# Optimization experiments

Hardware: AMD Instinct MI355X
Metric: run time of the kernel (lower is better)

## Reference

```python
import jax, jax.numpy as jnp
import numpy as np

# dims: heads, batch, seq (== maxSentenceSize), embed, key/query dim, value dim
H, B, S, E, DK, DV = 16, 4, 1024, 1024, 64, 64
SCALE = int(np.sqrt(DK))  # original uses int(np.sqrt(keySize)) == 8


def setup_inputs() -> dict:
    key = jax.random.key(0)
    k = jax.random.split(key, 5)
    embeddings = jax.random.normal(k[0], (B, S, E), jnp.float32)
    # original init: uniform(0, 1) weights
    Wq = jax.random.uniform(k[1], (H, E, DK), jnp.float32)
    Wk = jax.random.uniform(k[2], (H, E, DK), jnp.float32)
    # note: original valueWeights are also sized (E, keySize)
    Wv = jax.random.uniform(k[3], (H, E, DK), jnp.float32)
    Wo = jax.random.uniform(k[4], (H * DV, E), jnp.float32)
    return {"embeddings": embeddings, "Wq": Wq, "Wk": Wk, "Wv": Wv, "Wo": Wo}


def _causal_mask(s):
    # 0 on/below diagonal, -inf above (matches the torch list-comprehension mask)
    return jnp.where(jnp.tril(jnp.ones((s, s), bool)), 0.0, -jnp.inf).astype(jnp.float32)


def reference(embeddings, Wq, Wk, Wv, Wo):
    # per-head projections, all heads batched: [H,B,S,d]
    q = jnp.einsum('bse,hed->hbsd', embeddings, Wq)
    kk = jnp.einsum('bse,hed->hbsd', embeddings, Wk)
    v = jnp.einsum('bse,hed->hbsd', embeddings, Wv)
    # FAITHFUL to original: keys are RESHAPED (flat reinterpretation [S,DK]->[DK,S]
    # per (head,batch) slice), NOT transposed.
    kT = kk.reshape(H, B, DK, S)
    mask = _causal_mask(S)  # [S,S]
    # softmax((QK_reshaped + mask) / int(sqrt(keySize)))
    scores = (jnp.einsum('hbsd,hbdt->hbst', q, kT) + mask) / SCALE
    attn = jax.nn.softmax(scores, axis=-1)  # [H,B,S,S]
    av = jnp.einsum('hbst,hbtd->hbsd', attn, v)  # [H,B,S,DV]
    # FAITHFUL to original: flat reshape [H,B,S,DV] -> [B,S,DV*H]
    concat = av.reshape(B, S, DV * H)
    return concat @ Wo  # [B,S,E]
```

## Files before the change

### kernel.cpp

```cpp
#include <hip/hip_runtime.h>
#include <math.h>

#define H 16
#define B 4
#define S 1024
#define E 1024
#define DK 64

typedef _Float16 f16x8 __attribute__((ext_vector_type(8)));
typedef _Float16 f16x4 __attribute__((ext_vector_type(4)));
typedef float    f32x4 __attribute__((ext_vector_type(4)));

__device__ __forceinline__ int swzb(int row, int colByte) {
    return row * 128 + (colByte ^ ((row & 7) << 4));
}

__global__ __launch_bounds__(256) void cvt_split_emb(const float* __restrict__ in,
                                                     _Float16* __restrict__ outH,
                                                     _Float16* __restrict__ outL) {
    int i = (blockIdx.x * 256 + threadIdx.x) * 8;
    float4 a = *(const float4*)&in[i];
    float4 b = *(const float4*)&in[i + 4];
    float x[8] = {a.x, a.y, a.z, a.w, b.x, b.y, b.z, b.w};
    f16x8 h, l;
    #pragma unroll
    for (int j = 0; j < 8; ++j) {
        _Float16 hh = (_Float16)x[j];
        h[j] = hh;
        l[j] = (_Float16)(x[j] - (float)hh);
    }
    *(f16x8*)&outH[i] = h;
    *(f16x8*)&outL[i] = l;
}

__global__ __launch_bounds__(256) void cvt_weights(
    const float* __restrict__ Wq, const float* __restrict__ Wk,
    const float* __restrict__ Wv, const float* __restrict__ Wo,
    _Float16* __restrict__ WTh, _Float16* __restrict__ WTl,
    _Float16* __restrict__ WoT) {
    __shared__ _Float16 Th[64 * 64];
    __shared__ _Float16 Tl[64 * 64];
    int tid = threadIdx.x;
    if (blockIdx.y < 48) {
        int et = blockIdx.x, chunk = blockIdx.y;
        const float* W = (chunk < 16 ? Wq : chunk < 32 ? Wk : Wv)
                         + (size_t)(chunk & 15) * E * DK;
        #pragma unroll
        for (int rr = 0; rr < 4; ++rr) {
            int u = rr * 256 + tid;
            int ei = u >> 4, f4 = u & 15;
            float4 v = *(const float4*)&W[(size_t)(et * 64 + ei) * 64 + f4 * 4];
            float x[4] = {v.x, v.y, v.z, v.w};
            f16x4 h, l;
            #pragma unroll
            for (int j = 0; j < 4; ++j) {
                _Float16 hh = (_Float16)x[j];
                h[j] = hh;
                l[j] = (_Float16)(x[j] - (float)hh);
            }
            *(f16x4*)((char*)Th + swzb(ei, f4 * 8)) = h;
            *(f16x4*)((char*)Tl + swzb(ei, f4 * 8)) = l;
        }
        __syncthreads();
        #pragma unroll
        for (int rr = 0; rr < 2; ++rr) {
            int u = rr * 256 + tid;
            int d = u >> 3, e8 = u & 7;
            f16x8 oh, ol;
            #pragma unroll
            for (int j = 0; j < 8; ++j) {
                int ei = e8 * 8 + j;
                oh[j] = *(_Float16*)((char*)Th + swzb(ei, d * 2));
                ol[j] = *(_Float16*)((char*)Tl + swzb(ei, d * 2));
            }
            size_t idx = (size_t)(chunk * 64 + d) * 1024 + et * 64 + e8 * 8;
            *(f16x8*)&WTh[idx] = oh;
            if (chunk < 32) *(f16x8*)&WTl[idx] = ol;
        }
    } else {
        int kt = blockIdx.x, nt = blockIdx.y - 48;
        #pragma unroll
        for (int rr = 0; rr < 4; ++rr) {
            int u = rr * 256 + tid;
            int ki = u >> 4, f4 = u & 15;
            float4 v = *(const float4*)&Wo[(size_t)(kt * 64 + ki) * 1024 + nt * 64 + f4 * 4];
            f16x4 o = { (_Float16)v.x, (_Float16)v.y, (_Float16)v.z, (_Float16)v.w };
            *(f16x4*)((char*)Th + swzb(ki, f4 * 8)) = o;
        }
        __syncthreads();
        #pragma unroll
        for (int rr = 0; rr < 2; ++rr) {
            int u = rr * 256 + tid;
            int nl = u >> 3, k8 = u & 7;
            f16x8 o;
            #pragma unroll
            for (int j = 0; j < 8; ++j) {
                int ki = k8 * 8 + j;
                o[j] = *(_Float16*)((char*)Th + swzb(ki, nl * 2));
            }
            *(f16x8*)&WoT[(size_t)(nt * 64 + nl) * 1024 + kt * 64 + k8 * 8] = o;
        }
    }
}

__global__ __launch_bounds__(256) void gemm_qk(
    const _Float16* __restrict__ AH, const _Float16* __restrict__ AL,
    const _Float16* __restrict__ BTh, const _Float16* __restrict__ BTl,
    _Float16* __restrict__ QbH, _Float16* __restrict__ QbL,
    _Float16* __restrict__ kkTH, _Float16* __restrict__ kkTL) {
    __shared__ _Float16 AsH[128 * 32], AsL[128 * 32];
    __shared__ _Float16 BsH[128 * 32], BsL[128 * 32];
    int wg = ((int)blockIdx.x & 7) * 64 + ((int)blockIdx.x >> 3);
    int mt = wg >> 4, nt = wg & 15;
    int r0 = mt * 128, c0 = nt * 128;
    int tid = threadIdx.x, lane = tid & 63, w = tid >> 6;
    int wr = w >> 1, wc = w & 1;
    int l15 = lane & 15, l4 = lane >> 4;

    f32x4 zero = {0.f, 0.f, 0.f, 0.f};
    f32x4 acc[4][4];
    #pragma unroll
    for (int i = 0; i < 4; ++i)
        #pragma unroll
        for (int j = 0; j < 4; ++j) acc[i][j] = zero;

    for (int kt = 0; kt < 32; ++kt) {
        __syncthreads();
        #pragma unroll
        for (int rr = 0; rr < 2; ++rr) {
            int u = rr * 256 + tid;
            int row = u >> 2, c8 = u & 3;
            size_t ga = (size_t)(r0 + row) * 1024 + kt * 32 + c8 * 8;
            size_t gb = (size_t)(c0 + row) * 1024 + kt * 32 + c8 * 8;
            __builtin_amdgcn_global_load_lds(&AH[ga],  &AsH[u * 8], 16, 0, 0);
            __builtin_amdgcn_global_load_lds(&AL[ga],  &AsL[u * 8], 16, 0, 0);
            __builtin_amdgcn_global_load_lds(&BTh[gb], &BsH[u * 8], 16, 0, 0);
            __builtin_amdgcn_global_load_lds(&BTl[gb], &BsL[u * 8], 16, 0, 0);
        }
        __syncthreads();

        int kb = l4 * 16;
        f16x8 afH[4], afL[4], bfH[4], bfL[4];
        #pragma unroll
        for (int f = 0; f < 4; ++f) {
            int ar = wr * 64 + f * 16 + l15;
            int br = wc * 64 + f * 16 + l15;
            afH[f] = *(const f16x8*)((char*)AsH + ar * 64 + kb);
            afL[f] = *(const f16x8*)((char*)AsL + ar * 64 + kb);
            bfH[f] = *(const f16x8*)((char*)BsH + br * 64 + kb);
            bfL[f] = *(const f16x8*)((char*)BsL + br * 64 + kb);
        }
        #pragma unroll
        for (int i = 0; i < 4; ++i)
            #pragma unroll
            for (int j = 0; j < 4; ++j) {
                acc[i][j] = __builtin_amdgcn_mfma_f32_16x16x32_f16(
                    afH[i], bfH[j], acc[i][j], 0, 0, 0);
                acc[i][j] = __builtin_amdgcn_mfma_f32_16x16x32_f16(
                    afH[i], bfL[j], acc[i][j], 0, 0, 0);
                acc[i][j] = __builtin_amdgcn_mfma_f32_16x16x32_f16(
                    afL[i], bfH[j], acc[i][j], 0, 0, 0);
            }
    }

    #pragma unroll
    for (int i = 0; i < 4; ++i) {
        int grow0 = r0 + wr * 64 + i * 16 + l4 * 4;
        #pragma unroll
        for (int j = 0; j < 4; ++j) {
            int gcol = c0 + wc * 64 + j * 16 + l15;
            if (gcol < 1024) {
                int hh = gcol >> 6, dk = gcol & 63;
                #pragma unroll
                for (int r = 0; r < 4; ++r) {
                    int grow = grow0 + r;
                    int bb = grow >> 10, s = grow & 1023;
                    float v = acc[i][j][r];
                    _Float16 h = (_Float16)v;
                    size_t idx = (((size_t)hh * 4 + bb) * 1024 + s) * 64 + dk;
                    QbH[idx] = h;
                    QbL[idx] = (_Float16)(v - (float)h);
                }
            } else {
                int hh = (gcol >> 6) & 15, dk = gcol & 63;
                #pragma unroll
                for (int r = 0; r < 4; ++r) {
                    int grow = grow0 + r;
                    int bb = grow >> 10, s = grow & 1023;
                    float v = acc[i][j][r];
                    _Float16 h = (_Float16)v;
                    size_t idx = (((size_t)hh * 4 + bb) * 64 + (s >> 4)) * 1024
                                 + (s & 15) * 64 + dk;
                    kkTH[idx] = h;
                    kkTL[idx] = (_Float16)(v - (float)h);
                }
            }
        }
    }
}

__global__ __launch_bounds__(256) void gemm_v(
    const _Float16* __restrict__ AH, const _Float16* __restrict__ BTh,
    _Float16* __restrict__ V2) {
    __shared__ _Float16 As[128 * 32];
    __shared__ _Float16 Bs[64 * 32];
    int wg = ((int)blockIdx.x & 7) * 64 + ((int)blockIdx.x >> 3);
    int mt = wg >> 4, nt = wg & 15;
    int r0 = mt * 128, c0 = nt * 64;
    int tid = threadIdx.x, lane = tid & 63, w = tid >> 6;
    int wr = w >> 1, wc = w & 1;
    int l15 = lane & 15, l4 = lane >> 4;

    f32x4 zero = {0.f, 0.f, 0.f, 0.f};
    f32x4 acc[4][2];
    #pragma unroll
    for (int i = 0; i < 4; ++i)
        #pragma unroll
        for (int j = 0; j < 2; ++j) acc[i][j] = zero;

    for (int kt = 0; kt < 32; ++kt) {
        __syncthreads();
        #pragma unroll
        for (int rr = 0; rr < 2; ++rr) {
            int u = rr * 256 + tid;
            int row = u >> 2, c8 = u & 3;
            size_t ga = (size_t)(r0 + row) * 1024 + kt * 32 + c8 * 8;
            __builtin_amdgcn_global_load_lds(&AH[ga], &As[u * 8], 16, 0, 0);
        }
        {
            int u = tid;
            int row = u >> 2, c8 = u & 3;
            size_t gb = (size_t)(2048 + c0 + row) * 1024 + kt * 32 + c8 * 8;
            __builtin_amdgcn_global_load_lds(&BTh[gb], &Bs[u * 8], 16, 0, 0);
        }
        __syncthreads();

        int kb = l4 * 16;
        f16x8 af[4], bf[2];
        #pragma unroll
        for (int f = 0; f < 4; ++f) {
            int ar = wr * 64 + f * 16 + l15;
            af[f] = *(const f16x8*)((char*)As + ar * 64 + kb);
        }
        #pragma unroll
        for (int j = 0; j < 2; ++j) {
            int br = wc * 32 + j * 16 + l15;
            bf[j] = *(const f16x8*)((char*)Bs + br * 64 + kb);
        }
        #pragma unroll
        for (int i = 0; i < 4; ++i)
            #pragma unroll
            for (int j = 0; j < 2; ++j)
                acc[i][j] = __builtin_amdgcn_mfma_f32_16x16x32_f16(
                    af[i], bf[j], acc[i][j], 0, 0, 0);
    }

    #pragma unroll
    for (int i = 0; i < 4; ++i) {
        int grow0 = r0 + wr * 64 + i * 16 + l4 * 4;
        int bb = grow0 >> 10, s = grow0 & 1023;
        #pragma unroll
        for (int j = 0; j < 2; ++j) {
            int gcol = c0 + wc * 32 + j * 16 + l15;
            int hh = gcol >> 6, dv = gcol & 63;
            f16x4 o = { (_Float16)acc[i][j][0], (_Float16)acc[i][j][1],
                        (_Float16)acc[i][j][2], (_Float16)acc[i][j][3] };
            *(f16x4*)&V2[(((size_t)hh * 4 + bb) * 64 + dv) * 1024 + s] = o;
        }
    }
}

__global__ __launch_bounds__(256) void trans_k(const _Float16* __restrict__ kkTH,
                                               const _Float16* __restrict__ kkTL,
                                               _Float16* __restrict__ K2H,
                                               _Float16* __restrict__ K2L) {
    int tt = blockIdx.x;
    size_t hb = blockIdx.y;
    int mode = blockIdx.z;
    const _Float16* src = mode ? kkTL : kkTH;
    _Float16* dst = mode ? K2L : K2H;
    __shared__ _Float16 T[64 * 64];
    int tid = threadIdx.x;
    #pragma unroll
    for (int rr = 0; rr < 2; ++rr) {
        int u = rr * 256 + tid;
        int d = u >> 3, c8 = u & 7;
        f16x8 v = *(const f16x8*)&src[(hb * 64 + d) * 1024 + tt * 64 + c8 * 8];
        *(f16x8*)((char*)T + swzb(d, c8 * 16)) = v;
    }
    __syncthreads();
    #pragma unroll
    for (int rr = 0; rr < 2; ++rr) {
        int u = rr * 256 + tid;
        int ti = u >> 3, d8 = u & 7;
        f16x8 o;
        #pragma unroll
        for (int j = 0; j < 8; ++j)
            o[j] = *(_Float16*)((char*)T + swzb(d8 * 8 + j, ti * 2));
        *(f16x8*)&dst[(hb * 1024 + tt * 64 + ti) * 64 + d8 * 8] = o;
    }
}

__global__ __launch_bounds__(256) void attn(
    const _Float16* __restrict__ QbH, const _Float16* __restrict__ QbL,
    const _Float16* __restrict__ K2H, const _Float16* __restrict__ K2L,
    const _Float16* __restrict__ V2, _Float16* __restrict__ CC) {
    int qt = 15 - (int)blockIdx.x;
    int b = blockIdx.y, h = blockIdx.z;
    size_t hb = (size_t)h * 4 + b;
    __shared__ _Float16 QsH[64 * 64], QsL[64 * 64];
    __shared__ _Float16 KsH[64 * 64], KsL[64 * 64];
    __shared__ _Float16 Vs[64 * 64], Ps[64 * 64];
    int tid = threadIdx.x, lane = tid & 63, w = tid >> 6;
    int l15 = lane & 15, l4 = lane >> 4;
    int s0 = qt * 64;

    #pragma unroll
    for (int rr = 0; rr < 2; ++rr) {
        int u = rr * 256 + tid, row = u >> 3, c8 = u & 7;
        size_t gi = (hb * 1024 + s0 + row) * 64 + c8 * 8;
        int off = swzb(row, c8 * 16);
        *(f16x8*)((char*)QsH + off) = *(const f16x8*)&QbH[gi];
        *(f16x8*)((char*)QsL + off) = *(const f16x8*)&QbL[gi];
    }
    f16x8 rkH[2], rkL[2], rv[2];
    #pragma unroll
    for (int rr = 0; rr < 2; ++rr) {
        int u = rr * 256 + tid, row = u >> 3, c8 = u & 7;
        size_t ki = (hb * 1024 + row) * 64 + c8 * 8;
        rkH[rr] = *(const f16x8*)&K2H[ki];
        rkL[rr] = *(const f16x8*)&K2L[ki];
        rv[rr]  = *(const f16x8*)&V2[(hb * 64 + row) * 1024 + c8 * 8];
    }
    __syncthreads();
    int srow = w * 16 + l15;
    f16x8 qfH[2], qfL[2];
    #pragma unroll
    for (int ks = 0; ks < 2; ++ks) {
        int kb = (ks * 32 + l4 * 8) * 2;
        qfH[ks] = *(const f16x8*)((char*)QsH + swzb(srow, kb));
        qfL[ks] = *(const f16x8*)((char*)QsL + swzb(srow, kb));
    }

    float m = -__builtin_inff(), lsum = 0.f;
    f32x4 zero = {0.f, 0.f, 0.f, 0.f};
    f32x4 acc2[4] = {zero, zero, zero, zero};
    int sg = s0 + srow;
    int ntile = qt + 1;

    for (int tt = 0; tt < ntile; ++tt) {
        int t0 = tt * 64;
        __syncthreads();
        #pragma unroll
        for (int rr = 0; rr < 2; ++rr) {
            int u = rr * 256 + tid, row = u >> 3, c8 = u & 7;
            int off = swzb(row, c8 * 16);
            *(f16x8*)((char*)KsH + off) = rkH[rr];
            *(f16x8*)((char*)KsL + off) = rkL[rr];
            *(f16x8*)((char*)Vs + off)  = rv[rr];
        }
        if (tt + 1 < ntile) {
            int t0n = t0 + 64;
            #pragma unroll
            for (int rr = 0; rr < 2; ++rr) {
                int u = rr * 256 + tid, row = u >> 3, c8 = u & 7;
                size_t ki = (hb * 1024 + t0n + row) * 64 + c8 * 8;
                rkH[rr] = *(const f16x8*)&K2H[ki];
                rkL[rr] = *(const f16x8*)&K2L[ki];
                rv[rr]  = *(const f16x8*)&V2[(hb * 64 + row) * 1024 + t0n + c8 * 8];
            }
        }
        __syncthreads();

        f32x4 z[4] = {zero, zero, zero, zero};
        __builtin_amdgcn_s_setprio(1);
        #pragma unroll
        for (int ks = 0; ks < 2; ++ks) {
            int kb = (ks * 32 + l4 * 8) * 2;
            #pragma unroll
            for (int f = 0; f < 4; ++f) {
                int trow = f * 16 + l15;
                f16x8 akH = *(const f16x8*)((char*)KsH + swzb(trow, kb));
                f16x8 akL = *(const f16x8*)((char*)KsL + swzb(trow, kb));
                z[f] = __builtin_amdgcn_mfma_f32_16x16x32_f16(akH, qfH[ks], z[f], 0, 0, 0);
                z[f] = __builtin_amdgcn_mfma_f32_16x16x32_f16(akH, qfL[ks], z[f], 0, 0, 0);
                z[f] = __builtin_amdgcn_mfma_f32_16x16x32_f16(akL, qfH[ks], z[f], 0, 0, 0);
            }
        }
        __builtin_amdgcn_s_setprio(0);
        float mt = -__builtin_inff();
        #pragma unroll
        for (int f = 0; f < 4; ++f)
            #pragma unroll
            for (int r = 0; r < 4; ++r) {
                int tg = t0 + f * 16 + l4 * 4 + r;
                float val = z[f][r] * 0.125f;
                val = (tg > sg) ? -__builtin_inff() : val;
                z[f][r] = val;
                mt = fmaxf(mt, val);
            }
        mt = fmaxf(mt, __shfl_xor(mt, 16));
        mt = fmaxf(mt, __shfl_xor(mt, 32));
        float mn = fmaxf(m, mt);
        float corr = __expf(m - mn);
        float ps = 0.f;
        #pragma unroll
        for (int f = 0; f < 4; ++f)
            #pragma unroll
            for (int r = 0; r < 4; ++r) {
                float p = __expf(z[f][r] - mn);
                z[f][r] = p;
                ps += p;
            }
        ps += __shfl_xor(ps, 16);
        ps += __shfl_xor(ps, 32);
        lsum = lsum * corr + ps;
        m = mn;
        #pragma unroll
        for (int f = 0; f < 4; ++f) acc2[f] *= corr;

        #pragma unroll
        for (int f = 0; f < 4; ++f) {
            f16x4 pk = { (_Float16)z[f][0], (_Float16)z[f][1],
                         (_Float16)z[f][2], (_Float16)z[f][3] };
            *(f16x4*)((char*)Ps + swzb(srow, (f * 16 + l4 * 4) * 2)) = pk;
        }
        __builtin_amdgcn_s_setprio(1);
        #pragma unroll
        for (int ks = 0; ks < 2; ++ks) {
            int kb = (ks * 32 + l4 * 8) * 2;
            f16x8 bp = *(const f16x8*)((char*)Ps + swzb(srow, kb));
            #pragma unroll
            for (int f = 0; f < 4; ++f) {
                int dvrow = f * 16 + l15;
                f16x8 av = *(const f16x8*)((char*)Vs + swzb(dvrow, kb));
                acc2[f] = __builtin_amdgcn_mfma_f32_16x16x32_f16(av, bp, acc2[f], 0, 0, 0);
            }
        }
        __builtin_amdgcn_s_setprio(0);
    }

    float inv = 1.f / lsum;
    int sp = s0 + srow;
    int bprow = h >> 2;
    int spp = (h & 3) * 256 + b * 64 + (sp >> 4);
    int cb = (sp & 15) * 64;
    #pragma unroll
    for (int f = 0; f < 4; ++f) {
        int dv = f * 16 + l4 * 4;
        f16x4 o = { (_Float16)(acc2[f][0] * inv), (_Float16)(acc2[f][1] * inv),
                    (_Float16)(acc2[f][2] * inv), (_Float16)(acc2[f][3] * inv) };
        *(f16x4*)&CC[((size_t)bprow * 1024 + spp) * 1024 + cb + dv] = o;
    }
}

__global__ __launch_bounds__(256) void gemm_out(
    const _Float16* __restrict__ A, const _Float16* __restrict__ BT,
    float* __restrict__ out) {
    __shared__ _Float16 As[128 * 64];
    __shared__ _Float16 Bs[128 * 64];
    int wg = ((int)blockIdx.x & 7) * 32 + ((int)blockIdx.x >> 3);
    int mt = wg >> 3, nt = wg & 7;
    int r0 = mt * 128, c0 = nt * 128;
    int tid = threadIdx.x, lane = tid & 63, w = tid >> 6;
    int wr = w >> 1, wc = w & 1;
    int l15 = lane & 15, l4 = lane >> 4;

    f32x4 zero = {0.f, 0.f, 0.f, 0.f};
    f32x4 acc[4][4];
    #pragma unroll
    for (int i = 0; i < 4; ++i)
        #pragma unroll
        for (int j = 0; j < 4; ++j) acc[i][j] = zero;

    for (int kt = 0; kt < 16; ++kt) {
        __syncthreads();
        #pragma unroll
        for (int rr = 0; rr < 4; ++rr) {
            int u = rr * 256 + tid;
            int row = u >> 3, c8 = u & 7;
            size_t ga = (size_t)(r0 + row) * 1024 + kt * 64 + c8 * 8;
            size_t gb = (size_t)(c0 + row) * 1024 + kt * 64 + c8 * 8;
            __builtin_amdgcn_global_load_lds(&A[ga],  &As[u * 8], 16, 0, 0);
            __builtin_amdgcn_global_load_lds(&BT[gb], &Bs[u * 8], 16, 0, 0);
        }
        __syncthreads();

        #pragma unroll
        for (int ks = 0; ks < 2; ++ks) {
            int kb = (ks * 32 + l4 * 8) * 2;
            f16x8 af[4], bf[4];
            #pragma unroll
            for (int f = 0; f < 4; ++f) {
                int ar = wr * 64 + f * 16 + l15;
                int br = wc * 64 + f * 16 + l15;
                af[f] = *(const f16x8*)((char*)As + ar * 128 + kb);
                bf[f] = *(const f16x8*)((char*)Bs + br * 128 + kb);
            }
            #pragma unroll
            for (int i = 0; i < 4; ++i)
                #pragma unroll
                for (int j = 0; j < 4; ++j)
                    acc[i][j] = __builtin_amdgcn_mfma_f32_16x16x32_f16(
                        af[i], bf[j], acc[i][j], 0, 0, 0);
        }
    }

    #pragma unroll
    for (int i = 0; i < 4; ++i) {
        int grow0 = r0 + wr * 64 + i * 16 + l4 * 4;
        #pragma unroll
        for (int j = 0; j < 4; ++j) {
            int gcol = c0 + wc * 64 + j * 16 + l15;
            #pragma unroll
            for (int r = 0; r < 4; ++r)
                out[(size_t)(grow0 + r) * 1024 + gcol] = acc[i][j][r];
        }
    }
}

extern "C" void kernel_launch(void* const* d_in, const int* in_sizes, int n_in,
                              void* d_out, int out_size, void* d_ws, size_t ws_size,
                              hipStream_t stream) {
    const float* emb = (const float*)d_in[0];
    const float* Wq  = (const float*)d_in[1];
    const float* Wk  = (const float*)d_in[2];
    const float* Wv  = (const float*)d_in[3];
    const float* Wo  = (const float*)d_in[4];
    float* out = (float*)d_out;

    _Float16* embH = (_Float16*)d_ws;
    _Float16* embL = embH + 4194304;
    _Float16* WTh  = embL + 4194304;
    _Float16* WTl  = WTh + 3145728;
    _Float16* WoT  = WTl + 2097152;
    _Float16* QbH  = WoT + 1048576;
    _Float16* QbL  = QbH + 4194304;
    _Float16* V2   = QbL + 4194304;
    _Float16* K2H  = embH;
    _Float16* K2L  = embL;
    _Float16* CC   = WTh;
    _Float16* kkTH = (_Float16*)d_out;
    _Float16* kkTL = kkTH + 4194304;

    cvt_split_emb<<<2048, 256, 0, stream>>>(emb, embH, embL);
    cvt_weights  <<<dim3(16, 64), 256, 0, stream>>>(Wq, Wk, Wv, Wo, WTh, WTl, WoT);
    gemm_qk      <<<512, 256, 0, stream>>>(embH, embL, WTh, WTl, QbH, QbL, kkTH, kkTL);
    gemm_v       <<<512, 256, 0, stream>>>(embH, WTh, V2);
    trans_k      <<<dim3(16, 64, 2), 256, 0, stream>>>(kkTH, kkTL, K2H, K2L);
    attn         <<<dim3(16, 4, 16), 256, 0, stream>>>(QbH, QbL, K2H, K2L, V2, CC);
    gemm_out     <<<256, 256, 0, stream>>>(CC, WoT, out);
}
```

Baseline: 253.3 us.

## Fuse Q/K and V projection GEMMs into one launch with XOR-swizzled LDS tiles

Merges the split-precision Q/K projection GEMM and the V projection GEMM into a single 768-block kernel, with blocks branching on tile index. The V tiles grow to 128 columns, which gives more reuse. LDS tiles now use an XOR swizzle on the 16-byte chunk index, applied both in the global-to-LDS loads and in the fragment reads, to avoid bank conflicts. The same swizzle is applied to the output GEMM. The fused kernel saves one launch and lets the two workloads share the GPU, at the cost of uneven per-block work (32 vs 16 k-steps) and divergent code paths.

```diff
diff --git a/kernel.cpp b/kernel.cpp
--- a/kernel.cpp
+++ b/kernel.cpp
@@ -103,16 +103,17 @@
     }
 }
 
-__global__ __launch_bounds__(256) void gemm_qk(
+__global__ __launch_bounds__(256) void gemm_qkv(
     const _Float16* __restrict__ AH, const _Float16* __restrict__ AL,
     const _Float16* __restrict__ BTh, const _Float16* __restrict__ BTl,
     _Float16* __restrict__ QbH, _Float16* __restrict__ QbL,
-    _Float16* __restrict__ kkTH, _Float16* __restrict__ kkTL) {
-    __shared__ _Float16 AsH[128 * 32], AsL[128 * 32];
-    __shared__ _Float16 BsH[128 * 32], BsL[128 * 32];
-    int wg = ((int)blockIdx.x & 7) * 64 + ((int)blockIdx.x >> 3);
-    int mt = wg >> 4, nt = wg & 15;
-    int r0 = mt * 128, c0 = nt * 128;
+    _Float16* __restrict__ kkTH, _Float16* __restrict__ kkTL,
+    _Float16* __restrict__ V2) {
+    __shared__ _Float16 SA[128 * 64];
+    __shared__ _Float16 SB[128 * 64];
+    int wg = ((int)blockIdx.x & 7) * 96 + ((int)blockIdx.x >> 3);
+    int mt = wg / 24, nt = wg % 24;
+    int r0 = mt * 128;
     int tid = threadIdx.x, lane = tid & 63, w = tid >> 6;
     int wr = w >> 1, wc = w & 1;
     int l15 = lane & 15, l4 = lane >> 4;
@@ -124,148 +125,127 @@
         #pragma unroll
         for (int j = 0; j < 4; ++j) acc[i][j] = zero;
 
-    for (int kt = 0; kt < 32; ++kt) {
-        __syncthreads();
-        #pragma unroll
-        for (int rr = 0; rr < 2; ++rr) {
-            int u = rr * 256 + tid;
-            int row = u >> 2, c8 = u & 3;
-            size_t ga = (size_t)(r0 + row) * 1024 + kt * 32 + c8 * 8;
-            size_t gb = (size_t)(c0 + row) * 1024 + kt * 32 + c8 * 8;
-            __builtin_amdgcn_global_load_lds(&AH[ga],  &AsH[u * 8], 16, 0, 0);
-            __builtin_amdgcn_global_load_lds(&AL[ga],  &AsL[u * 8], 16, 0, 0);
-            __builtin_amdgcn_global_load_lds(&BTh[gb], &BsH[u * 8], 16, 0, 0);
-            __builtin_amdgcn_global_load_lds(&BTl[gb], &BsL[u * 8], 16, 0, 0);
-        }
-        __syncthreads();
-
-        int kb = l4 * 16;
-        f16x8 afH[4], afL[4], bfH[4], bfL[4];
-        #pragma unroll
-        for (int f = 0; f < 4; ++f) {
-            int ar = wr * 64 + f * 16 + l15;
-            int br = wc * 64 + f * 16 + l15;
-            afH[f] = *(const f16x8*)((char*)AsH + ar * 64 + kb);
-            afL[f] = *(const f16x8*)((char*)AsL + ar * 64 + kb);
-            bfH[f] = *(const f16x8*)((char*)BsH + br * 64 + kb);
-            bfL[f] = *(const f16x8*)((char*)BsL + br * 64 + kb);
-        }
-        #pragma unroll
-        for (int i = 0; i < 4; ++i)
+    if (nt < 16) {
+        int c0 = nt * 128;
+        for (int kt = 0; kt < 32; ++kt) {
+            __syncthreads();
+            #pragma unroll
+            for (int rr = 0; rr < 4; ++rr) {
+                int u = rr * 256 + tid;
+                int row = u >> 3, slot = u & 7;
+                int c = slot ^ (row & 7);
+                size_t kofs = (size_t)1024 * row + kt * 32 + (c & 3) * 8;
+                const _Float16* sa = (c < 4 ? AH : AL) + (size_t)r0 * 1024 + kofs;
+                const _Float16* sb = (c < 4 ? BTh : BTl) + (size_t)c0 * 1024 + kofs;
+                __builtin_amdgcn_global_load_lds(sa, &SA[u * 8], 16, 0, 0);
+                __builtin_amdgcn_global_load_lds(sb, &SB[u * 8], 16, 0, 0);
+            }
+            __syncthreads();
+
+            f16x8 afH[4], afL[4], bfH[4], bfL[4];
+            #pragma unroll
+            for (int f = 0; f < 4; ++f) {
+                int ar = wr * 64 + f * 16 + l15;
+                int br = wc * 64 + f * 16 + l15;
+                afH[f] = *(const f16x8*)((char*)SA + ar * 128 + ((l4    ) ^ (ar & 7)) * 16);
+                afL[f] = *(const f16x8*)((char*)SA + ar * 128 + ((l4 + 4) ^ (ar & 7)) * 16);
+                bfH[f] = *(const f16x8*)((char*)SB + br * 128 + ((l4    ) ^ (br & 7)) * 16);
+                bfL[f] = *(const f16x8*)((char*)SB + br * 128 + ((l4 + 4) ^ (br & 7)) * 16);
+            }
+            #pragma unroll
+            for (int i = 0; i < 4; ++i)
+                #pragma unroll
+                for (int j = 0; j < 4; ++j) {
+                    acc[i][j] = __builtin_amdgcn_mfma_f32_16x16x32_f16(
+                        afH[i], bfH[j], acc[i][j], 0, 0, 0);
+                    acc[i][j] = __builtin_amdgcn_mfma_f32_16x16x32_f16(
+                        afH[i], bfL[j], acc[i][j], 0, 0, 0);
+                    acc[i][j] = __builtin_amdgcn_mfma_f32_16x16x32_f16(
+                        afL[i], bfH[j], acc[i][j], 0, 0, 0);
+                }
+        }
+
+        #pragma unroll
+        for (int i = 0; i < 4; ++i) {
+            int grow0 = r0 + wr * 64 + i * 16 + l4 * 4;
             #pragma unroll
             for (int j = 0; j < 4; ++j) {
-                acc[i][j] = __builtin_amdgcn_mfma_f32_16x16x32_f16(
-                    afH[i], bfH[j], acc[i][j], 0, 0, 0);
-                acc[i][j] = __builtin_amdgcn_mfma_f32_16x16x32_f16(
-                    afH[i], bfL[j], acc[i][j], 0, 0, 0);
-                acc[i][j] = __builtin_amdgcn_mfma_f32_16x16x32_f16(
-                    afL[i], bfH[j], acc[i][j], 0, 0, 0);
-            }
-    }
-
-    #pragma unroll
-    for (int i = 0; i < 4; ++i) {
-        int grow0 = r0 + wr * 64 + i * 16 + l4 * 4;
-        #pragma unroll
-        for (int j = 0; j < 4; ++j) {
-            int gcol = c0 + wc * 64 + j * 16 + l15;
-            if (gcol < 1024) {
-                int hh = gcol >> 6, dk = gcol & 63;
+                int gcol = c0 + wc * 64 + j * 16 + l15;
+                if (gcol < 1024) {
+                    int hh = gcol >> 6, dk = gcol & 63;
+                    #pragma unroll
+                    for (int r = 0; r < 4; ++r) {
+                        int grow = grow0 + r;
+                        int bb = grow >> 10, s = grow & 1023;
+                        float v = acc[i][j][r];
+                        _Float16 h = (_Float16)v;
+                        size_t idx = (((size_t)hh * 4 + bb) * 1024 + s) * 64 + dk;
+                        QbH[idx] = h;
+                        QbL[idx] = (_Float16)(v - (float)h);
+                    }
+                } else {
+                    int hh = (gcol >> 6) & 15, dk = gcol & 63;
+                    #pragma unroll
+                    for (int r = 0; r < 4; ++r) {
+                        int grow = grow0 + r;
+                        int bb = grow >> 10, s = grow & 1023;
+                        float v = acc[i][j][r];
+                        _Float16 h = (_Float16)v;
+                        size_t idx = (((size_t)hh * 4 + bb) * 64 + (s >> 4)) * 1024
+                                     + (s & 15) * 64 + dk;
+                        kkTH[idx] = h;
+                        kkTL[idx] = (_Float16)(v - (float)h);
+                    }
+                }
+            }
+        }
+    } else {
+        int c0 = 2048 + (nt - 16) * 128;
+        for (int kt = 0; kt < 16; ++kt) {
+            __syncthreads();
+            #pragma unroll
+            for (int rr = 0; rr < 4; ++rr) {
+                int u = rr * 256 + tid;
+                int row = u >> 3, slot = u & 7;
+                int c = slot ^ (row & 7);
+                size_t ga = (size_t)(r0 + row) * 1024 + kt * 64 + c * 8;
+                size_t gb = (size_t)(c0 + row) * 1024 + kt * 64 + c * 8;
+                __builtin_amdgcn_global_load_lds(&AH[ga],  &SA[u * 8], 16, 0, 0);
+                __builtin_amdgcn_global_load_lds(&BTh[gb], &SB[u * 8], 16, 0, 0);
+            }
+            __syncthreads();
+
+            #pragma unroll
+            for (int ks = 0; ks < 2; ++ks) {
+                f16x8 af[4], bf[4];
                 #pragma unroll
-                for (int r = 0; r < 4; ++r) {
-                    int grow = grow0 + r;
-                    int bb = grow >> 10, s = grow & 1023;
-                    float v = acc[i][j][r];
-                    _Float16 h = (_Float16)v;
-                    size_t idx = (((size_t)hh * 4 + bb) * 1024 + s) * 64 + dk;
-                    QbH[idx] = h;
-                    QbL[idx] = (_Float16)(v - (float)h);
+                for (int f = 0; f < 4; ++f) {
+                    int ar = wr * 64 + f * 16 + l15;
+                    int br = wc * 64 + f * 16 + l15;
+                    af[f] = *(const f16x8*)((char*)SA + ar * 128 + ((ks * 4 + l4) ^ (ar & 7)) * 16);
+                    bf[f] = *(const f16x8*)((char*)SB + br * 128 + ((ks * 4 + l4) ^ (br & 7)) * 16);
                 }
-            } else {
-                int hh = (gcol >> 6) & 15, dk = gcol & 63;
                 #pragma unroll
-                for (int r = 0; r < 4; ++r) {
-                    int grow = grow0 + r;
-                    int bb = grow >> 10, s = grow & 1023;
-                    float v = acc[i][j][r];
-                    _Float16 h = (_Float16)v;
-                    size_t idx = (((size_t)hh * 4 + bb) * 64 + (s >> 4)) * 1024
-                                 + (s & 15) * 64 + dk;
-                    kkTH[idx] = h;
-                    kkTL[idx] = (_Float16)(v - (float)h);
-                }
-            }
-        }
-    }
-}
-
-__global__ __launch_bounds__(256) void gemm_v(
-    const _Float16* __restrict__ AH, const _Float16* __restrict__ BTh,
-    _Float16* __restrict__ V2) {
-    __shared__ _Float16 As[128 * 32];
-    __shared__ _Float16 Bs[64 * 32];
-    int wg = ((int)blockIdx.x & 7) * 64 + ((int)blockIdx.x >> 3);
-    int mt = wg >> 4, nt = wg & 15;
-    int r0 = mt * 128, c0 = nt * 64;
-    int tid = threadIdx.x, lane = tid & 63, w = tid >> 6;
-    int wr = w >> 1, wc = w & 1;
-    int l15 = lane & 15, l4 = lane >> 4;
-
-    f32x4 zero = {0.f, 0.f, 0.f, 0.f};
-    f32x4 acc[4][2];
-    #pragma unroll
-    for (int i = 0; i < 4; ++i)
-        #pragma unroll
-        for (int j = 0; j < 2; ++j) acc[i][j] = zero;
-
-    for (int kt = 0; kt < 32; ++kt) {
-        __syncthreads();
-        #pragma unroll
-        for (int rr = 0; rr < 2; ++rr) {
-            int u = rr * 256 + tid;
-            int row = u >> 2, c8 = u & 3;
-            size_t ga = (size_t)(r0 + row) * 1024 + kt * 32 + c8 * 8;
-            __builtin_amdgcn_global_load_lds(&AH[ga], &As[u * 8], 16, 0, 0);
-        }
-        {
-            int u = tid;
-            int row = u >> 2, c8 = u & 3;
-            size_t gb = (size_t)(2048 + c0 + row) * 1024 + kt * 32 + c8 * 8;
-            __builtin_amdgcn_global_load_lds(&BTh[gb], &Bs[u * 8], 16, 0, 0);
-        }
-        __syncthreads();
-
-        int kb = l4 * 16;
-        f16x8 af[4], bf[2];
-        #pragma unroll
-        for (int f = 0; f < 4; ++f) {
-            int ar = wr * 64 + f * 16 + l15;
-            af[f] = *(const f16x8*)((char*)As + ar * 64 + kb);
-        }
-        #pragma unroll
-        for (int j = 0; j < 2; ++j) {
-            int br = wc * 32 + j * 16 + l15;
-            bf[j] = *(const f16x8*)((char*)Bs + br * 64 + kb);
-        }
-        #pragma unroll
-        for (int i = 0; i < 4; ++i)
-            #pragma unroll
-            for (int j = 0; j < 2; ++j)
-                acc[i][j] = __builtin_amdgcn_mfma_f32_16x16x32_f16(
-                    af[i], bf[j], acc[i][j], 0, 0, 0);
-    }
-
-    #pragma unroll
-    for (int i = 0; i < 4; ++i) {
-        int grow0 = r0 + wr * 64 + i * 16 + l4 * 4;
-        int bb = grow0 >> 10, s = grow0 & 1023;
-        #pragma unroll
-        for (int j = 0; j < 2; ++j) {
-            int gcol = c0 + wc * 32 + j * 16 + l15;
-            int hh = gcol >> 6, dv = gcol & 63;
-            f16x4 o = { (_Float16)acc[i][j][0], (_Float16)acc[i][j][1],
-                        (_Float16)acc[i][j][2], (_Float16)acc[i][j][3] };
-            *(f16x4*)&V2[(((size_t)hh * 4 + bb) * 64 + dv) * 1024 + s] = o;
+                for (int i = 0; i < 4; ++i)
+                    #pragma unroll
+                    for (int j = 0; j < 4; ++j)
+                        acc[i][j] = __builtin_amdgcn_mfma_f32_16x16x32_f16(
+                            af[i], bf[j], acc[i][j], 0, 0, 0);
+            }
+        }
+
+        #pragma unroll
+        for (int i = 0; i < 4; ++i) {
+            int grow0 = r0 + wr * 64 + i * 16 + l4 * 4;
+            int bb = grow0 >> 10, s = grow0 & 1023;
+            #pragma unroll
+            for (int j = 0; j < 4; ++j) {
+                int gcol = c0 + wc * 64 + j * 16 + l15;
+                int hh = (gcol >> 6) & 15, dv = gcol & 63;
+                f16x4 o = { (_Float16)acc[i][j][0], (_Float16)acc[i][j][1],
+                            (_Float16)acc[i][j][2], (_Float16)acc[i][j][3] };
+                *(f16x4*)&V2[(((size_t)hh * 4 + bb) * 64 + dv) * 1024 + s] = o;
+            }
         }
     }
 }
@@ -478,9 +458,10 @@
         #pragma unroll
         for (int rr = 0; rr < 4; ++rr) {
             int u = rr * 256 + tid;
-            int row = u >> 3, c8 = u & 7;
-            size_t ga = (size_t)(r0 + row) * 1024 + kt * 64 + c8 * 8;
-            size_t gb = (size_t)(c0 + row) * 1024 + kt * 64 + c8 * 8;
+            int row = u >> 3, slot = u & 7;
+            int c = slot ^ (row & 7);
+            size_t ga = (size_t)(r0 + row) * 1024 + kt * 64 + c * 8;
+            size_t gb = (size_t)(c0 + row) * 1024 + kt * 64 + c * 8;
             __builtin_amdgcn_global_load_lds(&A[ga],  &As[u * 8], 16, 0, 0);
             __builtin_amdgcn_global_load_lds(&BT[gb], &Bs[u * 8], 16, 0, 0);
         }
@@ -488,14 +469,13 @@
 
         #pragma unroll
         for (int ks = 0; ks < 2; ++ks) {
-            int kb = (ks * 32 + l4 * 8) * 2;
             f16x8 af[4], bf[4];
             #pragma unroll
             for (int f = 0; f < 4; ++f) {
                 int ar = wr * 64 + f * 16 + l15;
                 int br = wc * 64 + f * 16 + l15;
-                af[f] = *(const f16x8*)((char*)As + ar * 128 + kb);
-                bf[f] = *(const f16x8*)((char*)Bs + br * 128 + kb);
+                af[f] = *(const f16x8*)((char*)As + ar * 128 + ((ks * 4 + l4) ^ (ar & 7)) * 16);
+                bf[f] = *(const f16x8*)((char*)Bs + br * 128 + ((ks * 4 + l4) ^ (br & 7)) * 16);
             }
             #pragma unroll
             for (int i = 0; i < 4; ++i)
@@ -545,8 +525,8 @@
 
     cvt_split_emb<<<2048, 256, 0, stream>>>(emb, embH, embL);
     cvt_weights  <<<dim3(16, 64), 256, 0, stream>>>(Wq, Wk, Wv, Wo, WTh, WTl, WoT);
-    gemm_qk      <<<512, 256, 0, stream>>>(embH, embL, WTh, WTl, QbH, QbL, kkTH, kkTL);
-    gemm_v       <<<512, 256, 0, stream>>>(embH, WTh, V2);
+    gemm_qkv     <<<768, 256, 0, stream>>>(embH, embL, WTh, WTl,
+                                           QbH, QbL, kkTH, kkTL, V2);
     trans_k      <<<dim3(16, 64, 2), 256, 0, stream>>>(kkTH, kkTL, K2H, K2L);
     attn         <<<dim3(16, 4, 16), 256, 0, stream>>>(QbH, QbL, K2H, K2L, V2, CC);
     gemm_out     <<<256, 256, 0, stream>>>(CC, WoT, out);
```

Measured after the change: 259.1 us. 1.02x slower.
